# Optimization experiments

Measured on AMD Instinct MI355X. Metric: run time of the kernel, lower is better.

The kernel has to match this reference:

```python
import jax, jax.numpy as jnp
import numpy as np
from jax import lax

N = 131072
E = 2097152
D = 128
B = 16
NC = 5
EPS = 1e-5


def setup_inputs() -> dict:
    key = jax.random.key(0)
    ks = jax.random.split(key, 32)
    inp = {
        'h': jax.random.normal(ks[0], (N, D), jnp.float32),
        'edge_w': jax.random.uniform(ks[1], (E,), jnp.float32),
        'src': jax.random.randint(ks[2], (E,), 0, N),
        'dst': jax.random.randint(ks[3], (E,), 0, N),
        'node_gid': jnp.sort(jax.random.randint(ks[4], (N,), 0, B)),
        'num_graphs': B,
    }
    s = 0.05
    inp['conv1_w'] = jax.random.normal(ks[5], (D, D, 3), jnp.float32) * s
    inp['conv1_b'] = jax.random.normal(ks[6], (D,), jnp.float32) * s
    inp['conv2_w'] = jax.random.normal(ks[7], (D, D, 3), jnp.float32) * s
    inp['conv2_b'] = jax.random.normal(ks[8], (D,), jnp.float32) * s
    inp['conv3_w'] = jax.random.normal(ks[9], (D, D, 3), jnp.float32) * s
    inp['conv3_b'] = jax.random.normal(ks[10], (D,), jnp.float32) * s
    inp['press_w'] = jax.random.normal(ks[11], (1, 3, 3), jnp.float32) * s
    inp['press_b'] = jax.random.normal(ks[12], (1,), jnp.float32) * s
    names = ['g11', 'g12', 'g13', 'g2', 'g3', 'g4']
    for i, nm in enumerate(names):
        inp[nm + '_w'] = jax.random.normal(ks[13 + 2 * i], (D, D), jnp.float32) * s
        inp[nm + '_b'] = jax.random.normal(ks[14 + 2 * i], (D,), jnp.float32) * s
    inp['bn_g'] = jnp.ones((D,), jnp.float32)
    inp['bn_b'] = jnp.zeros((D,), jnp.float32)
    inp['cls1_w'] = jax.random.normal(ks[25], (D, 3 * D), jnp.float32) * s
    inp['cls1_b'] = jax.random.normal(ks[26], (D,), jnp.float32) * s
    inp['cls2_w'] = jax.random.normal(ks[27], (NC, D), jnp.float32) * s
    inp['cls2_b'] = jax.random.normal(ks[28], (NC,), jnp.float32) * s
    return inp


def _conv1d_nodes(x, w, b, dil, pad):
    # x: [N, D] treated as a length-N 1D signal with D channels (as in original)
    y = lax.conv_general_dilated(x.T[None], w, window_strides=(1,),
                                 padding=[(pad, pad)], rhs_dilation=(dil,),
                                 dimension_numbers=('NCH', 'OIH', 'NCH'))
    return (y[0] + b[:, None]).T  # [N, D]


def _bn(x, g, b):
    mu = jnp.mean(x, axis=0)
    var = jnp.mean((x - mu) ** 2, axis=0)
    return (x - mu) * lax.rsqrt(var + EPS) * g + b


def _gconv(h, W, b, src, dst, ew, n):
    # DGL GraphConv norm='none': aggregate-first (in==out), msg = h[src]*ew, sum at dst, then @W + b
    msg = h[src] * ew[:, None]            # [E, D]
    agg = jax.ops.segment_sum(msg, dst, num_segments=n)
    return agg @ W + b


def reference(h, edge_w, src, dst, node_gid, num_graphs,
              conv1_w, conv1_b, conv2_w, conv2_b, conv3_w, conv3_b,
              press_w, press_b,
              g11_w, g11_b, g12_w, g12_b, g13_w, g13_b,
              g2_w, g2_b, g3_w, g3_b, g4_w, g4_b,
              bn_g, bn_b, cls1_w, cls1_b, cls2_w, cls2_b):
    n = h.shape[0]
    c1 = _conv1d_nodes(h, conv1_w, conv1_b, 1, 1)
    c2 = _conv1d_nodes(h, conv2_w, conv2_b, 2, 2)
    c3 = _conv1d_nodes(h, conv3_w, conv3_b, 3, 3)
    h01 = _bn(jax.nn.relu(c1) + c2, bn_g, bn_b)
    h02 = _bn(jax.nn.relu(c2) + c3, bn_g, bn_b)
    h03 = _bn(jax.nn.relu(c3) + c1, bn_g, bn_b)

    a1 = jax.nn.relu(_gconv(h01, g11_w, g11_b, src, dst, edge_w, n))
    a2 = jax.nn.relu(_gconv(h02, g12_w, g12_b, src, dst, edge_w, n))
    a3 = jax.nn.relu(_gconv(h03, g13_w, g13_b, src, dst, edge_w, n))
    stacked = jnp.stack([a1, a2, a3], axis=1)  # [N, 3, D]
    pressed = lax.conv_general_dilated(stacked, press_w, window_strides=(1,),
                                       padding=[(1, 1)],
                                       dimension_numbers=('NCH', 'OIH', 'NCH'))
    ac_h1 = pressed[:, 0, :] + press_b  # [N, D]
    ac_h1 = _bn(ac_h1, bn_g, bn_b)      # dropout is identity in eval

    ac_h2 = jax.nn.relu(_gconv(ac_h1, g2_w, g2_b, src, dst, edge_w, n))
    ac_h3 = jax.nn.relu(_gconv(ac_h2, g3_w, g3_b, src, dst, edge_w, n))
    ac_h4 = jax.nn.relu(_gconv(ac_h3, g4_w, g4_b, src, dst, edge_w, n))

    hg2 = jax.ops.segment_sum(ac_h2, node_gid, num_segments=num_graphs)
    hg3 = jax.ops.segment_sum(ac_h3, node_gid, num_segments=num_graphs)
    hg4 = jax.ops.segment_sum(ac_h4, node_gid, num_segments=num_graphs)
    hg = jnp.concatenate([hg2, hg3, hg4], axis=1)  # [B, 3D]
    out = (hg @ cls1_w.T + cls1_b) @ cls2_w.T + cls2_b  # [B, NC]
    return out
```

## Files before the change

kernel.cpp:

```cpp
#include <hip/hip_runtime.h>
#include <hip/hip_bf16.h>

#define NN 131072
#define EE 2097152
#define EPSS 1e-5f

typedef float f32x4 __attribute__((ext_vector_type(4)));
typedef short s16x8 __attribute__((ext_vector_type(8)));

static __device__ __forceinline__ ushort f2bf(float f) {
    uint u = __float_as_uint(f);
    u += 0x7fffu + ((u >> 16) & 1u);
    return (ushort)(u >> 16);
}
static __device__ __forceinline__ float bf2f(ushort h) {
    return __uint_as_float(((uint)h) << 16);
}


__global__ void dbg_kernel(float* __restrict__ out, float a, float b) {
    int i = threadIdx.x;
    if (i < 80) out[i] = (i == 0) ? a : ((i == 1) ? b : 0.f);
}


__global__ void hist_kernel(const int* __restrict__ dst, int* __restrict__ deg) {
    int e = blockIdx.x * 256 + threadIdx.x;
    if (e < EE) atomicAdd(&deg[dst[e]], 1);
}

__global__ __launch_bounds__(1024) void scanA_kernel(const int* __restrict__ deg,
                                                     int* __restrict__ rp,
                                                     int* __restrict__ bsum) {
    __shared__ int sh[1024];
    int t = threadIdx.x;
    int base = blockIdx.x * 1024;
    int v = deg[base + t];
    sh[t] = v;
    __syncthreads();
    for (int off = 1; off < 1024; off <<= 1) {
        int x = (t >= off) ? sh[t - off] : 0;
        __syncthreads();
        sh[t] += x;
        __syncthreads();
    }
    rp[base + t + 1] = sh[t];
    if (t == 1023) bsum[blockIdx.x] = sh[t];
}

__global__ __launch_bounds__(128) void scanB_kernel(int* __restrict__ bsum, int* __restrict__ boff) {
    __shared__ int sh[128];
    int t = threadIdx.x;
    int v = bsum[t];
    sh[t] = v;
    __syncthreads();
    for (int off = 1; off < 128; off <<= 1) {
        int x = (t >= off) ? sh[t - off] : 0;
        __syncthreads();
        sh[t] += x;
        __syncthreads();
    }
    boff[t] = sh[t] - v;
}

__global__ __launch_bounds__(1024) void scanC_kernel(int* __restrict__ rp, const int* __restrict__ boff) {
    int t = threadIdx.x;
    int b = blockIdx.x;
    rp[b * 1024 + t + 1] += boff[b];
    if (b == 0 && t == 0) rp[0] = 0;
}

__global__ void scatter_kernel(const int* __restrict__ src, const int* __restrict__ dst,
                               const float* __restrict__ ew, int* __restrict__ cur,
                               int2* __restrict__ ecw) {
    int e = blockIdx.x * 256 + threadIdx.x;
    if (e < EE) {
        int n = dst[e];
        int p = atomicAdd(&cur[n], 1);
        ecw[p] = make_int2(src[e], __float_as_int(ew[e]));
    }
}


__global__ void prepw_conv(const float* __restrict__ w1, const float* __restrict__ w2,
                           const float* __restrict__ w3, ushort* __restrict__ wTb) {
    int idx = blockIdx.x * 256 + threadIdx.x;
    if (idx >= 9 * 16384) return;
    int j = idx & 7;
    int lane = (idx >> 3) & 63;
    int ot = (idx >> 9) & 7;
    int kc = (idx >> 12) & 3;
    int ck = idx >> 14;
    int k = ck % 3, c = ck / 3;
    int i = kc * 32 + (lane >> 4) * 8 + j;
    int o = ot * 16 + (lane & 15);
    const float* w = (c == 0) ? w1 : ((c == 1) ? w2 : w3);
    wTb[idx] = f2bf(w[o * 384 + i * 3 + k]);
}

__global__ void prepw_g(const float* __restrict__ w0, const float* __restrict__ w1,
                        const float* __restrict__ w2, const float* __restrict__ w3,
                        const float* __restrict__ w4, const float* __restrict__ w5,
                        ushort* __restrict__ wGb) {
    int idx = blockIdx.x * 256 + threadIdx.x;
    if (idx >= 6 * 16384) return;
    int j = idx & 7;
    int lane = (idx >> 3) & 63;
    int ot = (idx >> 9) & 7;
    int kc = (idx >> 12) & 3;
    int m = idx >> 14;
    int i = kc * 32 + (lane >> 4) * 8 + j;
    int o = ot * 16 + (lane & 15);
    const float* w = (m == 0) ? w0 : ((m == 1) ? w1 : ((m == 2) ? w2 :
                     ((m == 3) ? w3 : ((m == 4) ? w4 : w5))));
    wGb[idx] = f2bf(w[i * 128 + o]);
}


__global__ __launch_bounds__(256) void conv_kernel(const float* __restrict__ h,
        const ushort* __restrict__ wTb,
        const float* __restrict__ b1, const float* __restrict__ b2, const float* __restrict__ b3,
        ushort* __restrict__ o1, ushort* __restrict__ o2, ushort* __restrict__ o3,
        float* __restrict__ stats) {
    __shared__ char smem[17920];
    __shared__ float red[768];
    int t = threadIdx.x;
    int n0 = blockIdx.x * 64;

    for (int idx = t; idx < 768; idx += 256) red[idx] = 0.f;

    for (int idx = t; idx < 70 * 32; idx += 256) {
        int row = idx >> 5, c4 = idx & 31;
        int gn = n0 - 3 + row;
        float4 v = make_float4(0.f, 0.f, 0.f, 0.f);
        if (gn >= 0 && gn < NN) v = *(const float4*)&h[(size_t)gn * 128 + c4 * 4];
        ushort4 pk;
        pk.x = f2bf(v.x); pk.y = f2bf(v.y); pk.z = f2bf(v.z); pk.w = f2bf(v.w);
        *(ushort4*)(smem + ((row * 256 + c4 * 8) ^ ((row & 7) << 4))) = pk;
    }
    __syncthreads();

    int wv = t >> 6, lane = t & 63;
    int fbase = lane & 15, grp = lane >> 4;
    int cbb = grp << 4;

    f32x4 acc[3][2][4];
#pragma unroll
    for (int c = 0; c < 3; c++)
#pragma unroll
        for (int o2 = 0; o2 < 2; o2++)
#pragma unroll
            for (int rg = 0; rg < 4; rg++) acc[c][o2][rg] = (f32x4){0.f, 0.f, 0.f, 0.f};

#pragma unroll
    for (int ck = 0; ck < 9; ck++) {
        const int c = ck / 3, k = ck % 3;
        const int shift = (c + 1) * (k - 1);
#pragma unroll
        for (int kc = 0; kc < 4; kc++) {
            s16x8 bA = *(const s16x8*)(wTb + (size_t)(((ck * 4 + kc) * 8 + wv * 2) * 512 + lane * 8));
            s16x8 bB = *(const s16x8*)(wTb + (size_t)(((ck * 4 + kc) * 8 + wv * 2 + 1) * 512 + lane * 8));
#pragma unroll
            for (int rg = 0; rg < 4; rg++) {
                int rr = rg * 16 + fbase + 3 + shift;
                s16x8 a = *(const s16x8*)(smem + ((rr * 256 + kc * 64 + cbb) ^ ((rr & 7) << 4)));
                acc[c][0][rg] = __builtin_amdgcn_mfma_f32_16x16x32_bf16(a, bA, acc[c][0][rg], 0, 0, 0);
                acc[c][1][rg] = __builtin_amdgcn_mfma_f32_16x16x32_bf16(a, bB, acc[c][1][rg], 0, 0, 0);
            }
        }
    }

    __syncthreads();

#pragma unroll
    for (int p = 0; p < 3; p++) {
        const int pa = p, pbx = (p + 1) % 3;
        const float* Ba = (p == 0) ? b1 : ((p == 1) ? b2 : b3);
        const float* Bb = (p == 0) ? b2 : ((p == 1) ? b3 : b1);
        ushort* Op = (p == 0) ? o1 : ((p == 1) ? o2 : o3);
#pragma unroll
        for (int o2 = 0; o2 < 2; o2++) {
            int f = (wv * 2 + o2) * 16 + fbase;
            float bba = Ba[f], bbb = Bb[f];
            float s = 0.f, ss = 0.f;
#pragma unroll
            for (int rg = 0; rg < 4; rg++) {
#pragma unroll
                for (int q = 0; q < 4; q++) {
                    float ca = acc[pa][o2][rg][q] + bba;
                    float cb = acc[pbx][o2][rg][q] + bbb;
                    float tv = fmaxf(ca, 0.f) + cb;
                    int nl = rg * 16 + grp * 4 + q;
                    *(ushort*)(smem + ((nl * 256 + f * 2) ^ ((nl & 7) << 4))) = f2bf(tv);
                    s += tv; ss += tv * tv;
                }
            }
            s  += __shfl_xor(s, 16);  s  += __shfl_xor(s, 32);
            ss += __shfl_xor(ss, 16); ss += __shfl_xor(ss, 32);
            if (lane < 16) {
                atomicAdd(&red[(2 * p) * 128 + f], s);
                atomicAdd(&red[(2 * p + 1) * 128 + f], ss);
            }
        }
        __syncthreads();
        for (int idx = t; idx < 1024; idx += 256) {
            int row = idx >> 4, c16 = idx & 15;
            uint4 v = *(const uint4*)(smem + ((row * 256 + c16 * 16) ^ ((row & 7) << 4)));
            *(uint4*)&Op[(size_t)(n0 + row) * 128 + c16 * 8] = v;
        }
        __syncthreads();
    }

    if (t < 128) {
#pragma unroll
        for (int p6 = 0; p6 < 6; p6++)
            atomicAdd(&stats[p6 * 128 + t], red[p6 * 128 + t]);
    }
}


__global__ __launch_bounds__(128) void bnfin_kernel(const float* __restrict__ stats,
                                                    const float* __restrict__ g,
                                                    const float* __restrict__ b,
                                                    float* __restrict__ scsh, int q0, int nq) {
    int d = threadIdx.x;
    for (int q = q0; q < q0 + nq; ++q) {
        float s  = stats[(2 * q) * 128 + d];
        float ss = stats[(2 * q + 1) * 128 + d];
        float mu  = s * (1.f / NN);
        float var = ss * (1.f / NN) - mu * mu;
        float sc = g[d] / sqrtf(var + EPSS);
        float sh = b[d] - mu * sc;
        scsh[q * 256 + d] = sc;
        scsh[q * 256 + 128 + d] = sh;
    }
}


__global__ __launch_bounds__(256) void gather_kernel(const ushort* __restrict__ xb,
        const int* __restrict__ rp, const int2* __restrict__ ecw,
        const float* __restrict__ scsh, ushort* __restrict__ G) {
    int t = threadIdx.x;
    int wid = blockIdx.x * 4 + (t >> 6);
    int lane = t & 63;
    uint laneoff = lane * 2;
    float scx = 1.f, scy = 1.f, shx = 0.f, shy = 0.f;
    if (scsh) {
        float2 sc = *(const float2*)&scsh[laneoff];
        float2 sh = *(const float2*)&scsh[128 + laneoff];
        scx = sc.x; scy = sc.y; shx = sh.x; shy = sh.y;
    }
    int beg = rp[wid], end = rp[wid + 1];
    int nb = (end - beg + 7) >> 3;
    float ax = 0.f, ay = 0.f, sw = 0.f;

    int2 ecb[8];
    if (nb > 0) {
#pragma unroll
        for (int q = 0; q < 8; q++) {
            int i = beg + q;
            int ic = (i < end) ? i : (end - 1);
            int2 v = ecw[ic];
            if (i >= end) v.y = 0;
            ecb[q] = v;
        }
    }
    for (int b = 0; b < nb; b++) {
        uint u[8];
#pragma unroll
        for (int q = 0; q < 8; q++)
            u[q] = *(const uint*)&xb[((uint)ecb[q].x << 7) + laneoff];

        int2 ecn[8];
        int e0n = beg + (b + 1) * 8;
#pragma unroll
        for (int q = 0; q < 8; q++) {
            int i = e0n + q;
            int ic = (i < end) ? i : (end - 1);
            int2 v = ecw[ic];
            if (i >= end) v.y = 0;
            ecn[q] = v;
        }
#pragma unroll
        for (int q = 0; q < 8; q++) {
            float w0 = __int_as_float(ecb[q].y);
            ax = fmaf(w0, __uint_as_float(u[q] << 16), ax);
            ay = fmaf(w0, __uint_as_float(u[q] & 0xffff0000u), ay);
            sw += w0;
        }
#pragma unroll
        for (int q = 0; q < 8; q++) ecb[q] = ecn[q];
    }

    if (scsh) {
        ax = fmaf(sw, shx, ax * scx);
        ay = fmaf(sw, shy, ay * scy);
    }
    uint pk = (uint)f2bf(ax) | ((uint)f2bf(ay) << 16);
    *(uint*)&G[(size_t)wid * 128 + laneoff] = pk;
}


__global__ __launch_bounds__(256) void gemm_kernel(const ushort* __restrict__ X,
        const ushort* __restrict__ wF, const float* __restrict__ bias,
        ushort* __restrict__ Y) {
    __shared__ char smem[16384];
    int t = threadIdx.x;
    int n0 = blockIdx.x * 64;
    int wv = t >> 6, lane = t & 63;

    s16x8 bfrag[4][2];
#pragma unroll
    for (int kc = 0; kc < 4; kc++)
#pragma unroll
        for (int o2 = 0; o2 < 2; o2++)
            bfrag[kc][o2] = *(const s16x8*)(wF + (size_t)((kc * 8 + wv * 2 + o2) * 512 + lane * 8));

    for (int idx = t; idx < 1024; idx += 256) {
        int row = idx >> 4, c16 = idx & 15;
        uint4 v = *(const uint4*)&X[(size_t)(n0 + row) * 128 + c16 * 8];
        *(uint4*)(smem + ((row * 256 + c16 * 16) ^ ((row & 7) << 4))) = v;
    }
    __syncthreads();

    int fbase = lane & 15, grp = lane >> 4, cbb = grp << 4;
    f32x4 acc[2][4];
#pragma unroll
    for (int o2 = 0; o2 < 2; o2++)
#pragma unroll
        for (int rg = 0; rg < 4; rg++) acc[o2][rg] = (f32x4){0.f, 0.f, 0.f, 0.f};

#pragma unroll
    for (int kc = 0; kc < 4; kc++) {
#pragma unroll
        for (int rg = 0; rg < 4; rg++) {
            int rr = rg * 16 + fbase;
            s16x8 a = *(const s16x8*)(smem + ((rr * 256 + kc * 64 + cbb) ^ ((rr & 7) << 4)));
            acc[0][rg] = __builtin_amdgcn_mfma_f32_16x16x32_bf16(a, bfrag[kc][0], acc[0][rg], 0, 0, 0);
            acc[1][rg] = __builtin_amdgcn_mfma_f32_16x16x32_bf16(a, bfrag[kc][1], acc[1][rg], 0, 0, 0);
        }
    }

    __syncthreads();
#pragma unroll
    for (int o2 = 0; o2 < 2; o2++) {
        int f = (wv * 2 + o2) * 16 + fbase;
        float bb = bias[f];
#pragma unroll
        for (int rg = 0; rg < 4; rg++)
#pragma unroll
            for (int q = 0; q < 4; q++) {
                float y = fmaxf(acc[o2][rg][q] + bb, 0.f);
                int nl = rg * 16 + grp * 4 + q;
                *(ushort*)(smem + ((nl * 256 + f * 2) ^ ((nl & 7) << 4))) = f2bf(y);
            }
    }
    __syncthreads();
    for (int idx = t; idx < 1024; idx += 256) {
        int row = idx >> 4, c16 = idx & 15;
        uint4 v = *(const uint4*)(smem + ((row * 256 + c16 * 16) ^ ((row & 7) << 4)));
        *(uint4*)&Y[(size_t)(n0 + row) * 128 + c16 * 8] = v;
    }
}


__global__ __launch_bounds__(256) void press_kernel(const ushort* __restrict__ a1,
                                                    const ushort* __restrict__ a2,
                                                    const ushort* __restrict__ a3,
                                                    const float* __restrict__ pw,
                                                    const float* __restrict__ pb_,
                                                    ushort* __restrict__ out,
                                                    float* __restrict__ stats) {
    __shared__ float rows[6 * 128];
    __shared__ float red[512];
    int t = threadIdx.x;
    int d = t & 127, r = t >> 7;
    int n0 = blockIdx.x * 64;
    float w[9];
#pragma unroll
    for (int q = 0; q < 9; q++) w[q] = pw[q];
    float pb = pb_[0];

    float s = 0.f, ss = 0.f;
    for (int it = 0; it < 32; ++it) {
        int npair = n0 + it * 2;
#pragma unroll
        for (int q = 0; q < 3; q++) {
            int idx = q * 256 + t;
            int row = idx >> 7, col = idx & 127;
            int c = row >> 1, rr = row & 1;
            size_t off = (size_t)(npair + rr) * 128 + col;
            ushort v = (c == 0) ? a1[off] : ((c == 1) ? a2[off] : a3[off]);
            rows[row * 128 + col] = bf2f(v);
        }
        __syncthreads();
        const float* R1 = &rows[(0 + r) * 128];
        const float* R2 = &rows[(2 + r) * 128];
        const float* R3 = &rows[(4 + r) * 128];
        float m1 = (d > 0) ? R1[d - 1] : 0.f;
        float m2 = (d > 0) ? R2[d - 1] : 0.f;
        float m3 = (d > 0) ? R3[d - 1] : 0.f;
        float p1 = (d < 127) ? R1[d + 1] : 0.f;
        float p2 = (d < 127) ? R2[d + 1] : 0.f;
        float p3 = (d < 127) ? R3[d + 1] : 0.f;
        float v = pb;
        v = fmaf(w[0], m1, v); v = fmaf(w[1], R1[d], v); v = fmaf(w[2], p1, v);
        v = fmaf(w[3], m2, v); v = fmaf(w[4], R2[d], v); v = fmaf(w[5], p2, v);
        v = fmaf(w[6], m3, v); v = fmaf(w[7], R3[d], v); v = fmaf(w[8], p3, v);
        out[(size_t)(npair + r) * 128 + d] = f2bf(v);
        s += v; ss += v * v;
        __syncthreads();
    }
    red[t] = s; red[256 + t] = ss;
    __syncthreads();
    if (t < 128) {
        atomicAdd(&stats[6 * 128 + t], red[t] + red[t + 128]);
        atomicAdd(&stats[7 * 128 + t], red[256 + t] + red[256 + t + 128]);
    }
}


__global__ __launch_bounds__(256) void pool_kernel(const ushort* __restrict__ x2,
                                                   const ushort* __restrict__ x3,
                                                   const ushort* __restrict__ x4,
                                                   const int* __restrict__ gid,
                                                   float* __restrict__ hg) {
    int t = threadIdx.x;
    int d = t & 127, r = t >> 7;
    int n0 = blockIdx.x * 64;
    float a2 = 0.f, a3 = 0.f, a4 = 0.f;
    int g = gid[n0 + r];
    for (int it = 0; it < 32; ++it) {
        int n = n0 + it * 2 + r;
        int gn = gid[n];
        if (gn != g) {
            atomicAdd(&hg[g * 384 + d], a2);
            atomicAdd(&hg[g * 384 + 128 + d], a3);
            atomicAdd(&hg[g * 384 + 256 + d], a4);
            a2 = a3 = a4 = 0.f;
            g = gn;
        }
        size_t base = (size_t)n * 128 + d;
        a2 += bf2f(x2[base]); a3 += bf2f(x3[base]); a4 += bf2f(x4[base]);
    }
    atomicAdd(&hg[g * 384 + d], a2);
    atomicAdd(&hg[g * 384 + 128 + d], a3);
    atomicAdd(&hg[g * 384 + 256 + d], a4);
}


__global__ __launch_bounds__(128) void final_kernel(const float* __restrict__ hg,
                                                    const float* __restrict__ w1,
                                                    const float* __restrict__ b1,
                                                    const float* __restrict__ w2,
                                                    const float* __restrict__ b2,
                                                    float* __restrict__ out) {
    __shared__ float hgs[16 * 384];
    __shared__ float tmp[16 * 128];
    int t = threadIdx.x;
    for (int idx = t; idx < 16 * 384; idx += 128) hgs[idx] = hg[idx];
    __syncthreads();
    for (int g = 0; g < 16; ++g) {
        float acc = b1[t];
        for (int k = 0; k < 384; k++) acc = fmaf(hgs[g * 384 + k], w1[t * 384 + k], acc);
        tmp[g * 128 + t] = acc;
    }
    __syncthreads();
    if (t < 80) {
        int g = t / 5, c = t % 5;
        float acc = b2[c];
        for (int j = 0; j < 128; j++) acc = fmaf(tmp[g * 128 + j], w2[c * 128 + j], acc);
        out[g * 5 + c] = acc;
    }
}


extern "C" void kernel_launch(void* const* d_in, const int* in_sizes, int n_in,
                              void* d_out, int out_size, void* d_ws, size_t ws_size,
                              hipStream_t stream) {
    (void)in_sizes; (void)n_in; (void)out_size;

    const float* h        = (const float*)d_in[0];
    const float* edge_w   = (const float*)d_in[1];
    const int*   src      = (const int*)d_in[2];
    const int*   dst      = (const int*)d_in[3];
    const int*   node_gid = (const int*)d_in[4];
    const float* c1w = (const float*)d_in[6];
    const float* c1b = (const float*)d_in[7];
    const float* c2w = (const float*)d_in[8];
    const float* c2b = (const float*)d_in[9];
    const float* c3w = (const float*)d_in[10];
    const float* c3b = (const float*)d_in[11];
    const float* pw  = (const float*)d_in[12];
    const float* pb  = (const float*)d_in[13];
    const float* g11w = (const float*)d_in[14];
    const float* g11b = (const float*)d_in[15];
    const float* g12w = (const float*)d_in[16];
    const float* g12b = (const float*)d_in[17];
    const float* g13w = (const float*)d_in[18];
    const float* g13b = (const float*)d_in[19];
    const float* g2w = (const float*)d_in[20];
    const float* g2b = (const float*)d_in[21];
    const float* g3w = (const float*)d_in[22];
    const float* g3b = (const float*)d_in[23];
    const float* g4w = (const float*)d_in[24];
    const float* g4b = (const float*)d_in[25];
    const float* bng = (const float*)d_in[26];
    const float* bnb = (const float*)d_in[27];
    const float* cls1w = (const float*)d_in[28];
    const float* cls1b = (const float*)d_in[29];
    const float* cls2w = (const float*)d_in[30];
    const float* cls2b = (const float*)d_in[31];

    const size_t NW = (size_t)NN * 128;
    ushort* U1 = (ushort*)d_ws;
    ushort* U2 = U1 + NW;
    ushort* U3 = U2 + NW;
    ushort* U4 = U3 + NW;
    ushort* G  = U4 + NW;
    int2*   ecw = (int2*)(G + NW);
    float*  stats = (float*)(ecw + EE);
    float*  scsh  = stats + 1024;
    ushort* wTb   = (ushort*)(scsh + 1024);
    ushort* wGb   = wTb + 9 * 16384;
    float*  hg    = (float*)(wGb + 6 * 16384);
    int*    rp    = (int*)(hg + 16 * 384);
    int*    cur   = rp + (NN + 1);
    int*    deg   = cur + NN;
    int*    bsum  = deg + NN;
    int*    boff  = bsum + 128;
    size_t required = (size_t)((char*)(boff + 128) - (char*)d_ws);

    if (ws_size < required) {
        dbg_kernel<<<1, 128, 0, stream>>>((float*)d_out, (float)ws_size,
                                          (float)(ws_size >> 20));
        return;
    }

    hipMemsetAsync(deg, 0, (size_t)NN * 4, stream);
    hipMemsetAsync(stats, 0, 1024 * 4, stream);
    hipMemsetAsync(hg, 0, (size_t)16 * 384 * 4, stream);

    hist_kernel<<<EE / 256, 256, 0, stream>>>(dst, deg);
    scanA_kernel<<<128, 1024, 0, stream>>>(deg, rp, bsum);
    scanB_kernel<<<1, 128, 0, stream>>>(bsum, boff);
    scanC_kernel<<<128, 1024, 0, stream>>>(rp, boff);
    hipMemcpyAsync(cur, rp, (size_t)NN * 4, hipMemcpyDeviceToDevice, stream);
    scatter_kernel<<<EE / 256, 256, 0, stream>>>(src, dst, edge_w, cur, ecw);

    prepw_conv<<<576, 256, 0, stream>>>(c1w, c2w, c3w, wTb);
    prepw_g<<<384, 256, 0, stream>>>(g11w, g12w, g13w, g2w, g3w, g4w, wGb);

    conv_kernel<<<NN / 64, 256, 0, stream>>>(h, wTb, c1b, c2b, c3b, U1, U2, U3, stats);
    bnfin_kernel<<<1, 128, 0, stream>>>(stats, bng, bnb, scsh, 0, 3);

    gather_kernel<<<NN / 4, 256, 0, stream>>>(U1, rp, ecw, scsh + 0 * 256, G);
    gemm_kernel<<<NN / 64, 256, 0, stream>>>(G, wGb + 0 * 16384, g11b, U4);
    gather_kernel<<<NN / 4, 256, 0, stream>>>(U2, rp, ecw, scsh + 1 * 256, G);
    gemm_kernel<<<NN / 64, 256, 0, stream>>>(G, wGb + 1 * 16384, g12b, U1);
    gather_kernel<<<NN / 4, 256, 0, stream>>>(U3, rp, ecw, scsh + 2 * 256, G);
    gemm_kernel<<<NN / 64, 256, 0, stream>>>(G, wGb + 2 * 16384, g13b, U2);

    press_kernel<<<NN / 64, 256, 0, stream>>>(U4, U1, U2, pw, pb, U3, stats);
    bnfin_kernel<<<1, 128, 0, stream>>>(stats, bng, bnb, scsh, 3, 1);

    gather_kernel<<<NN / 4, 256, 0, stream>>>(U3, rp, ecw, scsh + 3 * 256, G);
    gemm_kernel<<<NN / 64, 256, 0, stream>>>(G, wGb + 3 * 16384, g2b, U4);
    gather_kernel<<<NN / 4, 256, 0, stream>>>(U4, rp, ecw, nullptr, G);
    gemm_kernel<<<NN / 64, 256, 0, stream>>>(G, wGb + 4 * 16384, g3b, U1);
    gather_kernel<<<NN / 4, 256, 0, stream>>>(U1, rp, ecw, nullptr, G);
    gemm_kernel<<<NN / 64, 256, 0, stream>>>(G, wGb + 5 * 16384, g4b, U2);

    pool_kernel<<<NN / 64, 256, 0, stream>>>(U4, U1, U2, node_gid, hg);
    final_kernel<<<1, 128, 0, stream>>>(hg, cls1w, cls1b, cls2w, cls2b, (float*)d_out);
}
```

Before: 1.273 ms.

## Two-pass bucketed CSR build, fused triple gather, wider gather batches

Replaces the per-edge global-atomic scatter with a two-pass binning scheme. Edges are first grouped into 512 coarse buckets of 256 destination nodes using shared-memory histograms, then placed within each bucket using shared atomics, so the writes become more local. The three independent first-layer gathers are fused into one kernel that reads each edge record once and loads from all three feature arrays. The single gather now processes 16 edges per batch without explicit prefetching. The cost is extra workspace for three G buffers and a temporary edge array, and more register pressure in the fused gather.

```diff
diff --git a/kernel.cpp b/kernel.cpp
--- a/kernel.cpp
+++ b/kernel.cpp
@@ -3,6 +3,7 @@
 
 #define NN 131072
 #define EE 2097152
+#define NBK 512
 #define EPSS 1e-5f
 
 typedef float f32x4 __attribute__((ext_vector_type(4)));
@@ -70,14 +71,53 @@
     if (b == 0 && t == 0) rp[0] = 0;
 }
 
-__global__ void scatter_kernel(const int* __restrict__ src, const int* __restrict__ dst,
-                               const float* __restrict__ ew, int* __restrict__ cur,
-                               int2* __restrict__ ecw) {
-    int e = blockIdx.x * 256 + threadIdx.x;
-    if (e < EE) {
-        int n = dst[e];
-        int p = atomicAdd(&cur[n], 1);
-        ecw[p] = make_int2(src[e], __float_as_int(ew[e]));
+__global__ void initgb_kernel(const int* __restrict__ rp, int* __restrict__ gbkt) {
+    int t = blockIdx.x * 256 + threadIdx.x;
+    if (t < NBK) gbkt[t] = rp[t << 8];
+}
+
+__global__ __launch_bounds__(1024) void binA_kernel(const int* __restrict__ src,
+                                                    const int* __restrict__ dst,
+                                                    const float* __restrict__ ew,
+                                                    int* __restrict__ gbkt,
+                                                    int2* __restrict__ tmp) {
+    __shared__ int hist[NBK];
+    __shared__ int curs[NBK];
+    int t = threadIdx.x;
+    int e0 = blockIdx.x * 16384;
+    if (t < NBK) hist[t] = 0;
+    __syncthreads();
+#pragma unroll
+    for (int i = 0; i < 16; i++) {
+        int e = e0 + i * 1024 + t;
+        atomicAdd(&hist[dst[e] >> 8], 1);
+    }
+    __syncthreads();
+    if (t < NBK) curs[t] = atomicAdd(&gbkt[t], hist[t]);
+    __syncthreads();
+#pragma unroll
+    for (int i = 0; i < 16; i++) {
+        int e = e0 + i * 1024 + t;
+        int d = dst[e];
+        int p = atomicAdd(&curs[d >> 8], 1);
+        tmp[p] = make_int2(src[e] | ((d & 255) << 17), __float_as_int(ew[e]));
+    }
+}
+
+__global__ __launch_bounds__(256) void binB_kernel(const int* __restrict__ rp,
+                                                   const int2* __restrict__ tmp,
+                                                   int2* __restrict__ ecw) {
+    __shared__ int curs[256];
+    int t = threadIdx.x;
+    int nbase = blockIdx.x << 8;
+    curs[t] = rp[nbase + t];
+    __syncthreads();
+    int beg = rp[nbase], end = rp[nbase + 256];
+    for (int e = beg + t; e < end; e += 256) {
+        int2 v = tmp[e];
+        int dlow = (v.x >> 17) & 255;
+        int p = atomicAdd(&curs[dlow], 1);
+        ecw[p] = make_int2(v.x & 0x1FFFF, v.y);
     }
 }
 
@@ -237,67 +277,106 @@
 }
 
 
+__global__ __launch_bounds__(256) void gather3_kernel(const ushort* __restrict__ x1,
+        const ushort* __restrict__ x2, const ushort* __restrict__ x3,
+        const int* __restrict__ rp, const int2* __restrict__ ecw,
+        const float* __restrict__ scsh,
+        ushort* __restrict__ G1, ushort* __restrict__ G2, ushort* __restrict__ G3) {
+    int t = threadIdx.x;
+    int wid = blockIdx.x * 4 + (t >> 6);
+    int lane = t & 63;
+    uint lo = lane * 2;
+    float2 sc1 = *(const float2*)&scsh[lo],       sh1 = *(const float2*)&scsh[128 + lo];
+    float2 sc2 = *(const float2*)&scsh[256 + lo], sh2 = *(const float2*)&scsh[384 + lo];
+    float2 sc3 = *(const float2*)&scsh[512 + lo], sh3 = *(const float2*)&scsh[640 + lo];
+    int beg = rp[wid], end = rp[wid + 1];
+    float a1x = 0.f, a1y = 0.f, a2x = 0.f, a2y = 0.f, a3x = 0.f, a3y = 0.f, sw = 0.f;
+
+    for (int e0 = beg; e0 < end; e0 += 8) {
+        int2 rec[8];
+#pragma unroll
+        for (int q = 0; q < 8; q++) {
+            int i = e0 + q;
+            int ic = (i < end) ? i : (end - 1);
+            int2 v = ecw[ic];
+            if (i >= end) v.y = 0;
+            rec[q] = v;
+        }
+        uint u1[8], u2[8], u3[8];
+#pragma unroll
+        for (int q = 0; q < 8; q++) {
+            uint off = ((uint)rec[q].x << 7) + lo;
+            u1[q] = *(const uint*)&x1[off];
+            u2[q] = *(const uint*)&x2[off];
+            u3[q] = *(const uint*)&x3[off];
+        }
+#pragma unroll
+        for (int q = 0; q < 8; q++) {
+            float w = __int_as_float(rec[q].y);
+            a1x = fmaf(w, __uint_as_float(u1[q] << 16), a1x);
+            a1y = fmaf(w, __uint_as_float(u1[q] & 0xffff0000u), a1y);
+            a2x = fmaf(w, __uint_as_float(u2[q] << 16), a2x);
+            a2y = fmaf(w, __uint_as_float(u2[q] & 0xffff0000u), a2y);
+            a3x = fmaf(w, __uint_as_float(u3[q] << 16), a3x);
+            a3y = fmaf(w, __uint_as_float(u3[q] & 0xffff0000u), a3y);
+            sw += w;
+        }
+    }
+
+    a1x = fmaf(sw, sh1.x, a1x * sc1.x); a1y = fmaf(sw, sh1.y, a1y * sc1.y);
+    a2x = fmaf(sw, sh2.x, a2x * sc2.x); a2y = fmaf(sw, sh2.y, a2y * sc2.y);
+    a3x = fmaf(sw, sh3.x, a3x * sc3.x); a3y = fmaf(sw, sh3.y, a3y * sc3.y);
+    size_t base = (size_t)wid * 128 + lo;
+    *(uint*)&G1[base] = (uint)f2bf(a1x) | ((uint)f2bf(a1y) << 16);
+    *(uint*)&G2[base] = (uint)f2bf(a2x) | ((uint)f2bf(a2y) << 16);
+    *(uint*)&G3[base] = (uint)f2bf(a3x) | ((uint)f2bf(a3y) << 16);
+}
+
+
 __global__ __launch_bounds__(256) void gather_kernel(const ushort* __restrict__ xb,
         const int* __restrict__ rp, const int2* __restrict__ ecw,
         const float* __restrict__ scsh, ushort* __restrict__ G) {
     int t = threadIdx.x;
     int wid = blockIdx.x * 4 + (t >> 6);
     int lane = t & 63;
-    uint laneoff = lane * 2;
+    uint lo = lane * 2;
     float scx = 1.f, scy = 1.f, shx = 0.f, shy = 0.f;
     if (scsh) {
-        float2 sc = *(const float2*)&scsh[laneoff];
-        float2 sh = *(const float2*)&scsh[128 + laneoff];
+        float2 sc = *(const float2*)&scsh[lo];
+        float2 sh = *(const float2*)&scsh[128 + lo];
         scx = sc.x; scy = sc.y; shx = sh.x; shy = sh.y;
     }
     int beg = rp[wid], end = rp[wid + 1];
-    int nb = (end - beg + 7) >> 3;
     float ax = 0.f, ay = 0.f, sw = 0.f;
 
-    int2 ecb[8];
-    if (nb > 0) {
-#pragma unroll
-        for (int q = 0; q < 8; q++) {
-            int i = beg + q;
+    for (int e0 = beg; e0 < end; e0 += 16) {
+        int2 rec[16];
+#pragma unroll
+        for (int q = 0; q < 16; q++) {
+            int i = e0 + q;
             int ic = (i < end) ? i : (end - 1);
             int2 v = ecw[ic];
             if (i >= end) v.y = 0;
-            ecb[q] = v;
-        }
-    }
-    for (int b = 0; b < nb; b++) {
-        uint u[8];
-#pragma unroll
-        for (int q = 0; q < 8; q++)
-            u[q] = *(const uint*)&xb[((uint)ecb[q].x << 7) + laneoff];
-
-        int2 ecn[8];
-        int e0n = beg + (b + 1) * 8;
-#pragma unroll
-        for (int q = 0; q < 8; q++) {
-            int i = e0n + q;
-            int ic = (i < end) ? i : (end - 1);
-            int2 v = ecw[ic];
-            if (i >= end) v.y = 0;
-            ecn[q] = v;
-        }
-#pragma unroll
-        for (int q = 0; q < 8; q++) {
-            float w0 = __int_as_float(ecb[q].y);
-            ax = fmaf(w0, __uint_as_float(u[q] << 16), ax);
-            ay = fmaf(w0, __uint_as_float(u[q] & 0xffff0000u), ay);
-            sw += w0;
-        }
-#pragma unroll
-        for (int q = 0; q < 8; q++) ecb[q] = ecn[q];
+            rec[q] = v;
+        }
+        uint u[16];
+#pragma unroll
+        for (int q = 0; q < 16; q++)
+            u[q] = *(const uint*)&xb[((uint)rec[q].x << 7) + lo];
+#pragma unroll
+        for (int q = 0; q < 16; q++) {
+            float w = __int_as_float(rec[q].y);
+            ax = fmaf(w, __uint_as_float(u[q] << 16), ax);
+            ay = fmaf(w, __uint_as_float(u[q] & 0xffff0000u), ay);
+            sw += w;
+        }
     }
 
     if (scsh) {
         ax = fmaf(sw, shx, ax * scx);
         ay = fmaf(sw, shy, ay * scy);
     }
-    uint pk = (uint)f2bf(ax) | ((uint)f2bf(ay) << 16);
-    *(uint*)&G[(size_t)wid * 128 + laneoff] = pk;
+    *(uint*)&G[(size_t)wid * 128 + lo] = (uint)f2bf(ax) | ((uint)f2bf(ay) << 16);
 }
 
 
@@ -517,19 +596,22 @@
     ushort* U2 = U1 + NW;
     ushort* U3 = U2 + NW;
     ushort* U4 = U3 + NW;
-    ushort* G  = U4 + NW;
-    int2*   ecw = (int2*)(G + NW);
+    ushort* G1 = U4 + NW;
+    ushort* G2 = G1 + NW;
+    ushort* G3 = G2 + NW;
+    int2*   tmp = (int2*)G1;
+    int2*   ecw = (int2*)(G3 + NW);
     float*  stats = (float*)(ecw + EE);
     float*  scsh  = stats + 1024;
     ushort* wTb   = (ushort*)(scsh + 1024);
     ushort* wGb   = wTb + 9 * 16384;
     float*  hg    = (float*)(wGb + 6 * 16384);
     int*    rp    = (int*)(hg + 16 * 384);
-    int*    cur   = rp + (NN + 1);
-    int*    deg   = cur + NN;
+    int*    deg   = rp + (NN + 1);
     int*    bsum  = deg + NN;
     int*    boff  = bsum + 128;
-    size_t required = (size_t)((char*)(boff + 128) - (char*)d_ws);
+    int*    gbkt  = boff + 128;
+    size_t required = (size_t)((char*)(gbkt + NBK) - (char*)d_ws);
 
     if (ws_size < required) {
         dbg_kernel<<<1, 128, 0, stream>>>((float*)d_out, (float)ws_size,
@@ -545,8 +627,9 @@
     scanA_kernel<<<128, 1024, 0, stream>>>(deg, rp, bsum);
     scanB_kernel<<<1, 128, 0, stream>>>(bsum, boff);
     scanC_kernel<<<128, 1024, 0, stream>>>(rp, boff);
-    hipMemcpyAsync(cur, rp, (size_t)NN * 4, hipMemcpyDeviceToDevice, stream);
-    scatter_kernel<<<EE / 256, 256, 0, stream>>>(src, dst, edge_w, cur, ecw);
+    initgb_kernel<<<2, 256, 0, stream>>>(rp, gbkt);
+    binA_kernel<<<128, 1024, 0, stream>>>(src, dst, edge_w, gbkt, tmp);
+    binB_kernel<<<NBK, 256, 0, stream>>>(rp, tmp, ecw);
 
     prepw_conv<<<576, 256, 0, stream>>>(c1w, c2w, c3w, wTb);
     prepw_g<<<384, 256, 0, stream>>>(g11w, g12w, g13w, g2w, g3w, g4w, wGb);
@@ -554,22 +637,20 @@
     conv_kernel<<<NN / 64, 256, 0, stream>>>(h, wTb, c1b, c2b, c3b, U1, U2, U3, stats);
     bnfin_kernel<<<1, 128, 0, stream>>>(stats, bng, bnb, scsh, 0, 3);
 
-    gather_kernel<<<NN / 4, 256, 0, stream>>>(U1, rp, ecw, scsh + 0 * 256, G);
-    gemm_kernel<<<NN / 64, 256, 0, stream>>>(G, wGb + 0 * 16384, g11b, U4);
-    gather_kernel<<<NN / 4, 256, 0, stream>>>(U2, rp, ecw, scsh + 1 * 256, G);
-    gemm_kernel<<<NN / 64, 256, 0, stream>>>(G, wGb + 1 * 16384, g12b, U1);
-    gather_kernel<<<NN / 4, 256, 0, stream>>>(U3, rp, ecw, scsh + 2 * 256, G);
-    gemm_kernel<<<NN / 64, 256, 0, stream>>>(G, wGb + 2 * 16384, g13b, U2);
+    gather3_kernel<<<NN / 4, 256, 0, stream>>>(U1, U2, U3, rp, ecw, scsh, G1, G2, G3);
+    gemm_kernel<<<NN / 64, 256, 0, stream>>>(G1, wGb + 0 * 16384, g11b, U4);
+    gemm_kernel<<<NN / 64, 256, 0, stream>>>(G2, wGb + 1 * 16384, g12b, U1);
+    gemm_kernel<<<NN / 64, 256, 0, stream>>>(G3, wGb + 2 * 16384, g13b, U2);
 
     press_kernel<<<NN / 64, 256, 0, stream>>>(U4, U1, U2, pw, pb, U3, stats);
     bnfin_kernel<<<1, 128, 0, stream>>>(stats, bng, bnb, scsh, 3, 1);
 
-    gather_kernel<<<NN / 4, 256, 0, stream>>>(U3, rp, ecw, scsh + 3 * 256, G);
-    gemm_kernel<<<NN / 64, 256, 0, stream>>>(G, wGb + 3 * 16384, g2b, U4);
-    gather_kernel<<<NN / 4, 256, 0, stream>>>(U4, rp, ecw, nullptr, G);
-    gemm_kernel<<<NN / 64, 256, 0, stream>>>(G, wGb + 4 * 16384, g3b, U1);
-    gather_kernel<<<NN / 4, 256, 0, stream>>>(U1, rp, ecw, nullptr, G);
-    gemm_kernel<<<NN / 64, 256, 0, stream>>>(G, wGb + 5 * 16384, g4b, U2);
+    gather_kernel<<<NN / 4, 256, 0, stream>>>(U3, rp, ecw, scsh + 3 * 256, G2);
+    gemm_kernel<<<NN / 64, 256, 0, stream>>>(G2, wGb + 3 * 16384, g2b, U4);
+    gather_kernel<<<NN / 4, 256, 0, stream>>>(U4, rp, ecw, nullptr, G2);
+    gemm_kernel<<<NN / 64, 256, 0, stream>>>(G2, wGb + 4 * 16384, g3b, U1);
+    gather_kernel<<<NN / 4, 256, 0, stream>>>(U1, rp, ecw, nullptr, G2);
+    gemm_kernel<<<NN / 64, 256, 0, stream>>>(G2, wGb + 5 * 16384, g4b, U2);
 
     pool_kernel<<<NN / 64, 256, 0, stream>>>(U4, U1, U2, node_gid, hg);
     final_kernel<<<1, 128, 0, stream>>>(hg, cls1w, cls1b, cls2w, cls2b, (float*)d_out);
```

Result: slower. 1.300 ms (+2.2%).
